# Optimization experiments

Measured on AMD Instinct MI355X. Metric: run time of the kernel, lower is better.

## Reference

```python
import math
import jax, jax.numpy as jnp
import numpy as np

N_HEAD = 16
DIM = 1024
HEAD_DIM = DIM // N_HEAD  # 64


def _rope(x):
    # x: [b, h, t, d] ; lucidrains RotaryEmbedding default: interleaved pairs,
    # inv_freq = 1/theta^(2i/d), theta=10000, positions = arange(t)
    t, d = x.shape[2], x.shape[3]
    inv_freq = 1.0 / (10000.0 ** (jnp.arange(0, d, 2, dtype=jnp.float32) / d))  # [d/2]
    freqs = jnp.arange(t, dtype=jnp.float32)[:, None] * inv_freq[None, :]       # [t, d/2]
    emb = jnp.repeat(freqs, 2, axis=-1)                                          # [t, d]
    cos = jnp.cos(emb).astype(x.dtype)
    sin = jnp.sin(emb).astype(x.dtype)
    x1 = x[..., ::2]
    x2 = x[..., 1::2]
    rot = jnp.stack([-x2, x1], axis=-1).reshape(x.shape)  # rotate_half (interleaved)
    return x * cos + rot * sin


def setup_inputs() -> dict:
    key = jax.random.key(0)
    k1, k2, k3 = jax.random.split(key, 3)
    b, t = 2, 2048
    x = jax.random.normal(k1, (b, t, DIM), dtype=jnp.float32)
    w_qkv = jax.random.normal(k2, (DIM, 3 * DIM), dtype=jnp.float32) * (1.0 / math.sqrt(DIM))
    b_qkv = jnp.zeros((3 * DIM,), dtype=jnp.float32)
    w_out = jax.random.normal(k3, (DIM, DIM), dtype=jnp.float32) * (1.0 / math.sqrt(DIM))
    b_out = jnp.zeros((DIM,), dtype=jnp.float32)
    return {"x": x, "w_qkv": w_qkv, "b_qkv": b_qkv, "w_out": w_out, "b_out": b_out}


def reference(x, w_qkv, b_qkv, w_out, b_out):
    b, t, d = x.shape
    qkv = jnp.einsum('btd,de->bte', x, w_qkv) + b_qkv  # [b,t,3d]
    q, k, v = jnp.split(qkv, 3, axis=-1)
    # [b,t,d] -> [b,h,t,nd]
    def heads(z):
        return z.reshape(b, t, N_HEAD, HEAD_DIM).transpose(0, 2, 1, 3)
    q, k, v = heads(q), heads(k), heads(v)
    q = _rope(q)
    k = _rope(k)
    attn = jnp.einsum('bhqd,bhkd->bhqk', q, k) / math.sqrt(HEAD_DIM)
    attn = jax.nn.softmax(attn, axis=-1)
    # dropout is identity in eval mode
    out = jnp.einsum('bhqk,bhkd->bhqd', attn, v)
    out = out.transpose(0, 2, 1, 3).reshape(b, t, d)
    return jnp.einsum('btd,de->bte', out, w_out) + b_out
```

## Files before the change

### kernel.cpp

```cpp
#include <hip/hip_runtime.h>

typedef unsigned short u16;
typedef unsigned int u32;
typedef __attribute__((ext_vector_type(8))) short bf16x8;
typedef __attribute__((ext_vector_type(4))) float f32x4;
typedef __attribute__((ext_vector_type(16))) float f32x16;

typedef __attribute__((address_space(1))) const u32* gas_ptr;
typedef __attribute__((address_space(3))) u32* las_ptr;

__device__ __forceinline__ void gld16(const void* g, void* l) {
  __builtin_amdgcn_global_load_lds((gas_ptr)g, (las_ptr)l, 16, 0, 0);
}

__device__ __forceinline__ u16 f2bf(float f) {
  unsigned u = __float_as_uint(f);
  u = u + 0x7fffu + ((u >> 16) & 1u);
  return (u16)(u >> 16);
}

__global__ __launch_bounds__(256) void prep(const float* __restrict__ x, u16* __restrict__ x_bf,
                                            const float* __restrict__ wqkv, u16* __restrict__ wqkvT,
                                            const float* __restrict__ wout, u16* __restrict__ woutT,
                                            float2* __restrict__ cs) {
  __shared__ float tile[32][33];
  const int b = blockIdx.x, tid = threadIdx.x;
  if (b < 4096) {
    int i = b * 256 + tid;
    float4 v = reinterpret_cast<const float4*>(x)[i];
    ushort4 o = make_ushort4(f2bf(v.x), f2bf(v.y), f2bf(v.z), f2bf(v.w));
    reinterpret_cast<ushort4*>(x_bf)[i] = o;
  } else if (b < 8192) {
    const float* in; u16* out; int R, C, bx, by;
    if (b < 7168) { in = wqkv; out = wqkvT; R = 1024; C = 3072; int b2 = b - 4096; bx = b2 % 96; by = b2 / 96; }
    else          { in = wout; out = woutT; R = 1024; C = 1024; int b3 = b - 7168; bx = b3 % 32; by = b3 / 32; }
    int tx = tid & 31, ty = tid >> 5;
    int c0 = bx * 32, r0 = by * 32;
#pragma unroll
    for (int i = 0; i < 32; i += 8)
      tile[ty + i][tx] = in[(size_t)(r0 + ty + i) * C + c0 + tx];
    __syncthreads();
#pragma unroll
    for (int i = 0; i < 32; i += 8)
      out[(size_t)(c0 + ty + i) * R + r0 + tx] = f2bf(tile[tx][ty + i]);
  } else {
    int idx = (b - 8192) * 256 + tid;
    int i = idx & 31, t = idx >> 5;
    float invf = powf(10000.0f, -(float)(2 * i) / 64.0f);
    float f = (float)t * invf;
    cs[idx] = make_float2(cosf(f), sinf(f));
  }
}

#define BM 128
#define BN 128
#define BKK 32
__global__ __launch_bounds__(256) void gemm_bt(
    const u16* __restrict__ A, const u16* __restrict__ Bt, const float* __restrict__ bias,
    float* __restrict__ Cf, u16* __restrict__ q_ws, u16* __restrict__ k_ws, u16* __restrict__ v_ws,
    const float2* __restrict__ cs, int M, int N, int K, int mode) {
  __shared__ u16 As[BM][BKK];
  __shared__ u16 Bs[BN][BKK];
  const int tid = threadIdx.x;
  const int lane = tid & 63;
  const int wid = tid >> 6;
  const int wr = wid >> 1, wc = wid & 1;
  const int fr = lane & 15, fg = lane >> 4;
  const int m0 = blockIdx.y * BM, n0 = blockIdx.x * BN;

  const int row_l = lane >> 2;
  const int slot_l = lane & 3;

  f32x4 acc[4][4] = {};

  for (int k0 = 0; k0 < K; k0 += BKK) {
#pragma unroll
    for (int i = 0; i < 2; i++) {
      int rowA = wid * 32 + i * 16;
      gld16(A  + (size_t)(m0 + rowA + row_l) * K + k0 + slot_l * 8, &As[rowA][0]);
      gld16(Bt + (size_t)(n0 + rowA + row_l) * K + k0 + slot_l * 8, &Bs[rowA][0]);
    }
    __syncthreads();
    bf16x8 af[4], bfr[4];
#pragma unroll
    for (int i = 0; i < 4; i++)
      af[i] = *reinterpret_cast<const bf16x8*>(&As[wr * 64 + i * 16 + fr][fg * 8]);
#pragma unroll
    for (int j = 0; j < 4; j++)
      bfr[j] = *reinterpret_cast<const bf16x8*>(&Bs[wc * 64 + j * 16 + fr][fg * 8]);
#pragma unroll
    for (int i = 0; i < 4; i++)
#pragma unroll
      for (int j = 0; j < 4; j++)
        acc[i][j] = __builtin_amdgcn_mfma_f32_16x16x32_bf16(af[i], bfr[j], acc[i][j], 0, 0, 0);
    __syncthreads();
  }

#pragma unroll
  for (int i = 0; i < 4; i++) {
    int rowb = m0 + wr * 64 + i * 16 + fg * 4;
#pragma unroll
    for (int j = 0; j < 4; j++) {
      int col = n0 + wc * 64 + j * 16 + fr;
      float bv = bias[col];
#pragma unroll
      for (int r = 0; r < 4; r++) {
        float v = acc[i][j][r] + bv;
        int rr = rowb + r;
        if (mode == 0) {
          Cf[(size_t)rr * N + col] = v;
        } else {
          int b = rr >> 11, t = rr & 2047;
          int sec = col >> 10, nn = col & 1023;
          int h = nn >> 6, d = nn & 63;
          float vv = v;
          if (sec < 2) {
            float vp = __shfl_xor(v, 1);
            float2 c_s = cs[(t << 5) + (d >> 1)];
            vv = (d & 1) ? fmaf(v, c_s.x, vp * c_s.y) : fmaf(v, c_s.x, -vp * c_s.y);
          }
          size_t dst = ((size_t)((b << 4) + h) * 2048 + t) * 64 + d;
          u16 val = f2bf(vv);
          if (sec == 0) q_ws[dst] = val;
          else if (sec == 1) k_ws[dst] = val;
          else v_ws[dst] = val;
        }
      }
    }
  }
}

#define KVB 64
#define NT 32
#define CSC 0.18033688011112042f
#define THRL2 11.5415603f

__global__ __launch_bounds__(256, 2) void attn_fwd(const u16* __restrict__ q_ws,
                                                   const u16* __restrict__ k_ws,
                                                   const u16* __restrict__ v_ws,
                                                   u16* __restrict__ attn_out) {
  __shared__ u16 Klds[2][4096];
  __shared__ u16 Vlds[2][4096];

  const int tid = threadIdx.x, lane = tid & 63, w = tid >> 6;
  const int l31 = lane & 31, hi = lane >> 5;
  const int bid = blockIdx.x;
  const int wrk = (bid & 7) * 64 + (bid >> 3);
  const int bh = wrk >> 4;
  const int q0 = (wrk & 15) * 128 + w * 32;
  const size_t base = (size_t)bh * (2048 * 64);

  bf16x8 qf[4];
#pragma unroll
  for (int db = 0; db < 4; db++)
    qf[db] = *reinterpret_cast<const bf16x8*>(
        q_ws + base + (size_t)(q0 + l31) * 64 + db * 16 + hi * 8);

  f32x16 Oa[2] = {};
  float m_i = -1e30f, l_i = 0.f;

  const int krow_l = lane >> 3, kslot_l = lane & 7;
  const int vkey = tid & 31, vc = tid >> 5;
  const u16* kg = k_ws + base;
  const u16* vg = v_ws + base;

#define STAGE_K(kv, buf)                                                          \
  {                                                                               \
    _Pragma("unroll") for (int i = 0; i < 2; i++) {                               \
      int row = w * 16 + i * 8 + krow_l;                                          \
      int srcslot = kslot_l ^ (row & 7);                                          \
      gld16(kg + (size_t)((kv) + row) * 64 + srcslot * 8, &Klds[buf][(w * 16 + i * 8) * 64]); \
    }                                                                             \
  }
#define LOAD_V(kv, vrg)                                                           \
  {                                                                               \
    vrg[0] = *reinterpret_cast<const uint4*>(vg + (size_t)((kv) + vkey) * 64 + vc * 8);       \
    vrg[1] = *reinterpret_cast<const uint4*>(vg + (size_t)((kv) + vkey + 32) * 64 + vc * 8);  \
  }
#define SCATTER_V(vrg, buf)                                                       \
  {                                                                               \
    _Pragma("unroll") for (int it = 0; it < 2; it++) {                            \
      const u16* pe = (const u16*)&vrg[it];                                       \
      int key2 = (vkey + 32 * it) * 2;                                            \
      _Pragma("unroll") for (int j = 0; j < 8; j++) {                             \
        int byte = (vc * 8 + j) * 128 + (key2 ^ (j << 4));                        \
        *(u16*)((char*)&Vlds[buf][0] + byte) = pe[j];                             \
      }                                                                           \
    }                                                                             \
  }

  uint4 vr[2];
  STAGE_K(0, 0);
  LOAD_V(0, vr);
  __syncthreads();
  SCATTER_V(vr, 0);
  __syncthreads();

  int cur = 0;
  for (int t = 0; t < NT; t++) {
    if (t + 1 < NT) {
      STAGE_K((t + 1) * KVB, cur ^ 1);
      LOAD_V((t + 1) * KVB, vr);
    }

    const char* Kb = (const char*)&Klds[cur][0];
    const char* Vb = (const char*)&Vlds[cur][0];

    bf16x8 kf[2][4];
#pragma unroll
    for (int ks = 0; ks < 2; ks++) {
      int krow = (l31 + 32 * ks) * 128;
      int ksw = (l31 & 7) << 4;
#pragma unroll
      for (int db = 0; db < 4; db++)
        kf[ks][db] = *reinterpret_cast<const bf16x8*>(Kb + krow + ((db * 32 + hi * 16) ^ ksw));
    }

    f32x16 s0 = {}, s1 = {};
    __builtin_amdgcn_s_setprio(1);
#pragma unroll
    for (int db = 0; db < 4; db++) {
      s0 = __builtin_amdgcn_mfma_f32_32x32x16_bf16(kf[0][db], qf[db], s0, 0, 0, 0);
      s1 = __builtin_amdgcn_mfma_f32_32x32x16_bf16(kf[1][db], qf[db], s1, 0, 0, 0);
    }
    __builtin_amdgcn_s_setprio(0);

    float a[8];
#pragma unroll
    for (int i = 0; i < 8; i++)
      a[i] = fmaxf(fmaxf(s0[i], s0[i + 8]), fmaxf(s1[i], s1[i + 8]));
    a[0] = fmaxf(a[0], a[4]); a[1] = fmaxf(a[1], a[5]);
    a[2] = fmaxf(a[2], a[6]); a[3] = fmaxf(a[3], a[7]);
    float zx = fmaxf(fmaxf(a[0], a[1]), fmaxf(a[2], a[3])) * CSC;
    zx = fmaxf(zx, __shfl_xor(zx, 32));

    if (__any(zx > m_i + THRL2)) {
      float mn = fmaxf(m_i, zx);
      float alpha = exp2f(m_i - mn);
      m_i = mn;
      l_i *= alpha;
#pragma unroll
      for (int ds = 0; ds < 2; ds++)
#pragma unroll
        for (int r = 0; r < 16; r++) Oa[ds][r] *= alpha;
    }

    float p[32];
#pragma unroll
    for (int i = 0; i < 16; i++) {
      p[i]      = exp2f(fmaf(s0[i], CSC, -m_i));
      p[16 + i] = exp2f(fmaf(s1[i], CSC, -m_i));
    }
    float r0 = 0.f, r1 = 0.f, r2 = 0.f, r3 = 0.f;
#pragma unroll
    for (int i = 0; i < 8; i++) {
      r0 += p[i]; r1 += p[i + 8]; r2 += p[i + 16]; r3 += p[i + 24];
    }
    float rs = (r0 + r1) + (r2 + r3);
    rs += __shfl_xor(rs, 32);
    l_i += rs;

    u32 pw[16];
#pragma unroll
    for (int kk = 0; kk < 2; kk++)
#pragma unroll
      for (int wd = 0; wd < 8; wd++)
        pw[kk * 8 + wd] =
            ((u32)f2bf(p[kk * 16 + 2 * wd + 1]) << 16) | (u32)f2bf(p[kk * 16 + 2 * wd]);

    int vsw = (l31 & 7) << 4;
    __builtin_amdgcn_s_setprio(1);
#pragma unroll
    for (int ds = 0; ds < 2; ds++) {
      int vrow = (l31 + 32 * ds) * 128;
#pragma unroll
      for (int kb = 0; kb < 4; kb++) {
        uint2 va = *(const uint2*)(Vb + vrow + ((kb * 32 + hi * 8) ^ vsw));
        uint2 vb2 = *(const uint2*)(Vb + vrow + ((kb * 32 + hi * 8 + 16) ^ vsw));
        union { u32 u[4]; bf16x8 v; } vf, pf;
        vf.u[0] = va.x; vf.u[1] = va.y; vf.u[2] = vb2.x; vf.u[3] = vb2.y;
        int pb = (kb >> 1) * 8 + (kb & 1) * 4;
        pf.u[0] = pw[pb]; pf.u[1] = pw[pb + 1]; pf.u[2] = pw[pb + 2]; pf.u[3] = pw[pb + 3];
        Oa[ds] = __builtin_amdgcn_mfma_f32_32x32x16_bf16(vf.v, pf.v, Oa[ds], 0, 0, 0);
      }
    }
    __builtin_amdgcn_s_setprio(0);

    if (t + 1 < NT) SCATTER_V(vr, cur ^ 1);
    __syncthreads();
    cur ^= 1;
  }

  const int b = bh >> 4, h = bh & 15;
  float invl = 1.0f / l_i;
  int row = q0 + l31;
  size_t rbase = ((size_t)(b * 2048 + row)) * 1024 + h * 64;
#pragma unroll
  for (int ds = 0; ds < 2; ds++)
#pragma unroll
    for (int rg = 0; rg < 4; rg++) {
      int d0 = rg * 8 + hi * 4 + ds * 32;
      ushort4 st;
      st.x = f2bf(Oa[ds][rg * 4 + 0] * invl);
      st.y = f2bf(Oa[ds][rg * 4 + 1] * invl);
      st.z = f2bf(Oa[ds][rg * 4 + 2] * invl);
      st.w = f2bf(Oa[ds][rg * 4 + 3] * invl);
      *reinterpret_cast<ushort4*>(attn_out + rbase + d0) = st;
    }
#undef STAGE_K
#undef LOAD_V
#undef SCATTER_V
}

extern "C" void kernel_launch(void* const* d_in, const int* in_sizes, int n_in,
                              void* d_out, int out_size, void* d_ws, size_t ws_size,
                              hipStream_t stream) {
  const float* x     = (const float*)d_in[0];
  const float* w_qkv = (const float*)d_in[1];
  const float* b_qkv = (const float*)d_in[2];
  const float* w_out = (const float*)d_in[3];
  const float* b_out = (const float*)d_in[4];
  float* out = (float*)d_out;

  char* ws = (char*)d_ws;
  const size_t MB = 1024 * 1024;
  u16*    x_bf   = (u16*)(ws);
  u16*    wqkvT  = (u16*)(ws + 8 * MB);
  u16*    woutT  = (u16*)(ws + 14 * MB);
  u16*    q_ws   = (u16*)(ws + 16 * MB);
  u16*    k_ws   = (u16*)(ws + 24 * MB);
  u16*    v_ws   = (u16*)(ws + 32 * MB);
  u16*    attn_o = (u16*)(ws + 40 * MB);
  float2* cs     = (float2*)(ws + 48 * MB);

  prep<<<8448, 256, 0, stream>>>(x, x_bf, w_qkv, wqkvT, w_out, woutT, cs);
  gemm_bt<<<dim3(24, 32), 256, 0, stream>>>(x_bf, wqkvT, b_qkv, nullptr, q_ws, k_ws, v_ws,
                                            cs, 4096, 3072, 1024, 1);
  attn_fwd<<<512, 256, 0, stream>>>(q_ws, k_ws, v_ws, attn_o);
  gemm_bt<<<dim3(8, 32), 256, 0, stream>>>(attn_o, woutT, b_out, out, nullptr, nullptr, nullptr,
                                           nullptr, 4096, 1024, 1024, 0);
}
```

Before: 244.6 us.

## Write V transposed from QKV GEMM and stage it via direct global-to-LDS loads

After: 249.6 us. 1.02x slower.

```diff
diff --git a/kernel.cpp b/kernel.cpp
--- a/kernel.cpp
+++ b/kernel.cpp
@@ -1,4 +1,5 @@
 #include <hip/hip_runtime.h>
+#include <hip/hip_bf16.h>
 
 typedef unsigned short u16;
 typedef unsigned int u32;
@@ -103,27 +104,33 @@
     for (int j = 0; j < 4; j++) {
       int col = n0 + wc * 64 + j * 16 + fr;
       float bv = bias[col];
-#pragma unroll
-      for (int r = 0; r < 4; r++) {
-        float v = acc[i][j][r] + bv;
-        int rr = rowb + r;
-        if (mode == 0) {
-          Cf[(size_t)rr * N + col] = v;
+      if (mode == 0) {
+#pragma unroll
+        for (int r = 0; r < 4; r++)
+          Cf[(size_t)(rowb + r) * N + col] = acc[i][j][r] + bv;
+      } else {
+        int bb = rowb >> 11, t0 = rowb & 2047;
+        int sec = col >> 10, nn = col & 1023;
+        int h = nn >> 6, d = nn & 63;
+        int bh = (bb << 4) + h;
+        if (sec == 2) {
+          ushort4 st;
+          st.x = f2bf(acc[i][j][0] + bv);
+          st.y = f2bf(acc[i][j][1] + bv);
+          st.z = f2bf(acc[i][j][2] + bv);
+          st.w = f2bf(acc[i][j][3] + bv);
+          *reinterpret_cast<ushort4*>(v_ws + ((size_t)(bh * 64 + d)) * 2048 + t0) = st;
         } else {
-          int b = rr >> 11, t = rr & 2047;
-          int sec = col >> 10, nn = col & 1023;
-          int h = nn >> 6, d = nn & 63;
-          float vv = v;
-          if (sec < 2) {
+          u16* dst = (sec == 0) ? q_ws : k_ws;
+#pragma unroll
+          for (int r = 0; r < 4; r++) {
+            float v = acc[i][j][r] + bv;
             float vp = __shfl_xor(v, 1);
+            int t = t0 + r;
             float2 c_s = cs[(t << 5) + (d >> 1)];
-            vv = (d & 1) ? fmaf(v, c_s.x, vp * c_s.y) : fmaf(v, c_s.x, -vp * c_s.y);
+            float vv = (d & 1) ? fmaf(v, c_s.x, vp * c_s.y) : fmaf(v, c_s.x, -vp * c_s.y);
+            dst[((size_t)bh * 2048 + t) * 64 + d] = f2bf(vv);
           }
-          size_t dst = ((size_t)((b << 4) + h) * 2048 + t) * 64 + d;
-          u16 val = f2bf(vv);
-          if (sec == 0) q_ws[dst] = val;
-          else if (sec == 1) k_ws[dst] = val;
-          else v_ws[dst] = val;
         }
       }
     }
@@ -160,9 +167,8 @@
   float m_i = -1e30f, l_i = 0.f;
 
   const int krow_l = lane >> 3, kslot_l = lane & 7;
-  const int vkey = tid & 31, vc = tid >> 5;
   const u16* kg = k_ws + base;
-  const u16* vg = v_ws + base;
+  const u16* vgT = v_ws + base;
 
 #define STAGE_K(kv, buf)                                                          \
   {                                                                               \
@@ -172,35 +178,24 @@
       gld16(kg + (size_t)((kv) + row) * 64 + srcslot * 8, &Klds[buf][(w * 16 + i * 8) * 64]); \
     }                                                                             \
   }
-#define LOAD_V(kv, vrg)                                                           \
+#define STAGE_V(kv, buf)                                                          \
   {                                                                               \
-    vrg[0] = *reinterpret_cast<const uint4*>(vg + (size_t)((kv) + vkey) * 64 + vc * 8);       \
-    vrg[1] = *reinterpret_cast<const uint4*>(vg + (size_t)((kv) + vkey + 32) * 64 + vc * 8);  \
-  }
-#define SCATTER_V(vrg, buf)                                                       \
-  {                                                                               \
-    _Pragma("unroll") for (int it = 0; it < 2; it++) {                            \
-      const u16* pe = (const u16*)&vrg[it];                                       \
-      int key2 = (vkey + 32 * it) * 2;                                            \
-      _Pragma("unroll") for (int j = 0; j < 8; j++) {                             \
-        int byte = (vc * 8 + j) * 128 + (key2 ^ (j << 4));                        \
-        *(u16*)((char*)&Vlds[buf][0] + byte) = pe[j];                             \
-      }                                                                           \
+    _Pragma("unroll") for (int i = 0; i < 2; i++) {                               \
+      int row = w * 16 + i * 8 + krow_l;                             \
+      int srcslot = kslot_l ^ (row & 7);                                          \
+      gld16(vgT + (size_t)row * 2048 + (kv) + srcslot * 8, &Vlds[buf][(w * 16 + i * 8) * 64]); \
     }                                                                             \
   }
 
-  uint4 vr[2];
   STAGE_K(0, 0);
-  LOAD_V(0, vr);
-  __syncthreads();
-  SCATTER_V(vr, 0);
+  STAGE_V(0, 0);
   __syncthreads();
 
   int cur = 0;
   for (int t = 0; t < NT; t++) {
     if (t + 1 < NT) {
       STAGE_K((t + 1) * KVB, cur ^ 1);
-      LOAD_V((t + 1) * KVB, vr);
+      STAGE_V((t + 1) * KVB, cur ^ 1);
     }
 
     const char* Kb = (const char*)&Klds[cur][0];
@@ -264,9 +259,13 @@
 #pragma unroll
     for (int kk = 0; kk < 2; kk++)
 #pragma unroll
-      for (int wd = 0; wd < 8; wd++)
-        pw[kk * 8 + wd] =
-            ((u32)f2bf(p[kk * 16 + 2 * wd + 1]) << 16) | (u32)f2bf(p[kk * 16 + 2 * wd]);
+      for (int wd = 0; wd < 8; wd++) {
+        __hip_bfloat162 hh =
+            __float22bfloat162_rn(make_float2(p[kk * 16 + 2 * wd], p[kk * 16 + 2 * wd + 1]));
+        u32 uu;
+        __builtin_memcpy(&uu, &hh, 4);
+        pw[kk * 8 + wd] = uu;
+      }
 
     int vsw = (l31 & 7) << 4;
     __builtin_amdgcn_s_setprio(1);
@@ -286,7 +285,6 @@
     }
     __builtin_amdgcn_s_setprio(0);
 
-    if (t + 1 < NT) SCATTER_V(vr, cur ^ 1);
     __syncthreads();
     cur ^= 1;
   }
@@ -308,8 +306,7 @@
       *reinterpret_cast<ushort4*>(attn_out + rbase + d0) = st;
     }
 #undef STAGE_K
-#undef LOAD_V
-#undef SCATTER_V
+#undef STAGE_V
 }
 
 extern "C" void kernel_launch(void* const* d_in, const int* in_sizes, int n_in,
```
